# Kernel tuning notes

Hardware: AMD Instinct MI355X
Metric: run time of the kernel (lower is better)

## Reference

```python
import jax, jax.numpy as jnp
import numpy as np

B, S, H, D = 4, 2048, 16, 64
DM = H * D  # d_model = 1024


def setup_inputs() -> dict:
    key = jax.random.key(0)
    ks = jax.random.split(key, 11)
    s = 1.0 / np.sqrt(DM)
    return {
        "query": jax.random.normal(ks[0], (B, S, DM), jnp.float32),
        "key": jax.random.normal(ks[1], (B, S, DM), jnp.float32),
        "value": jax.random.normal(ks[2], (B, S, DM), jnp.float32),
        "Wq": jax.random.uniform(ks[3], (DM, DM), jnp.float32, -s, s),
        "bq": jax.random.uniform(ks[4], (DM,), jnp.float32, -s, s),
        "Wk": jax.random.uniform(ks[5], (DM, DM), jnp.float32, -s, s),
        "bk": jax.random.uniform(ks[6], (DM,), jnp.float32, -s, s),
        "Wv": jax.random.uniform(ks[7], (DM, DM), jnp.float32, -s, s),
        "bv": jax.random.uniform(ks[8], (DM,), jnp.float32, -s, s),
        "Wo": jax.random.uniform(ks[9], (DM, DM), jnp.float32, -s, s),
        "bo": jax.random.uniform(ks[10], (DM,), jnp.float32, -s, s),
        "masking": 1,
    }


def reference(query, key, value, Wq, bq, Wk, bk, Wv, bv, Wo, bo, masking):
    b, s, _ = query.shape
    # Linear projections (torch Linear: x @ W.T + b), split into heads
    q = (query @ Wq.T + bq).reshape(b, s, H, D).transpose(0, 2, 1, 3)  # [B,H,S,D]
    k = (key @ Wk.T + bk).reshape(b, -1, H, D).transpose(0, 2, 1, 3)
    v = (value @ Wv.T + bv).reshape(b, -1, H, D).transpose(0, 2, 1, 3)
    scores = jnp.einsum("bhqd,bhkd->bhqk", q, k) / np.power(D, 0.5)
    if masking:
        # subsequent (strictly upper-triangular) mask -> fill with -1e9
        sub = jnp.triu(jnp.ones((s, k.shape[2]), bool), k=1)
        scores = jnp.where(sub, jnp.float32(-1e9), scores)
    attn = jax.nn.softmax(scores, axis=-1)
    out = jnp.einsum("bhqk,bhkd->bhqd", attn, v)  # [B,H,S,D]
    out = out.transpose(0, 2, 1, 3).reshape(b, s, H * D)
    return out @ Wo.T + bo
```

## Files before the change

### kernel.cpp

```cpp
#include <hip/hip_runtime.h>
#include <stdint.h>
#include <stddef.h>

#define B_ 4
#define S_ 2048
#define H_ 16
#define D_ 64
#define DM 1024
#define MTOT 8192

typedef __bf16 bf16x8 __attribute__((ext_vector_type(8)));
typedef __bf16 bf16x4 __attribute__((ext_vector_type(4)));
typedef float  f32x4  __attribute__((ext_vector_type(4)));

__device__ __forceinline__ void g2l16(const void* g, void* l) {
  __builtin_amdgcn_global_load_lds(
      (__attribute__((address_space(1))) void*)g,
      (__attribute__((address_space(3))) void*)l, 16, 0, 0);
}

__global__ __launch_bounds__(256) void cvt_kernel(const float* __restrict__ src,
                                                  __bf16* __restrict__ dst, int n4) {
  int i = blockIdx.x * 256 + threadIdx.x;
  if (i < n4) {
    const float4 v = ((const float4*)src)[i];
    bf16x4 o;
    o.x = (__bf16)v.x; o.y = (__bf16)v.y; o.z = (__bf16)v.z; o.w = (__bf16)v.w;
    ((bf16x4*)dst)[i] = o;
  }
}

struct QKVArgs {
  const __bf16 *A0, *A1, *A2;
  const __bf16 *W0, *W1, *W2;
  const float *b0, *b1, *b2;
  __bf16 *oQ, *oK, *oVt;
};

__global__ __launch_bounds__(256) void gemm_qkv(QKVArgs args) {
  const int z = blockIdx.z;
  const __bf16* A    = (z == 0) ? args.A0 : (z == 1) ? args.A1 : args.A2;
  const __bf16* W    = (z == 0) ? args.W0 : (z == 1) ? args.W1 : args.W2;
  const float*  bias = (z == 0) ? args.b0 : (z == 1) ? args.b1 : args.b2;

  __shared__ __bf16 As[128 * 32];
  __shared__ __bf16 Bs[128 * 32];

  const int m0 = blockIdx.x * 128;
  const int n0 = blockIdx.y * 128;
  const int tid = threadIdx.x;
  const int wave = tid >> 6, lane = tid & 63;
  const int lrow = lane & 15, lhi = lane >> 4;
  const int moff = (wave & 1) * 64, noff = (wave >> 1) * 64;
  const int srow = lane >> 2;
  const int schunk = (lane & 3) * 8;

  f32x4 acc[4][4] = {};

  for (int k0 = 0; k0 < DM; k0 += 32) {
#pragma unroll
    for (int p = 0; p < 2; ++p) {
      const int rg = (p * 4 + wave) * 16;
      g2l16(A + (size_t)(m0 + rg + srow) * DM + k0 + schunk, As + rg * 32 + lane * 8);
      g2l16(W + (size_t)(n0 + rg + srow) * DM + k0 + schunk, Bs + rg * 32 + lane * 8);
    }
    __syncthreads();
    bf16x8 af[4], bfr[4];
#pragma unroll
    for (int i = 0; i < 4; ++i) {
      af[i]  = *(const bf16x8*)(As + (moff + i * 16 + lrow) * 32 + lhi * 8);
      bfr[i] = *(const bf16x8*)(Bs + (noff + i * 16 + lrow) * 32 + lhi * 8);
    }
#pragma unroll
    for (int i = 0; i < 4; ++i)
#pragma unroll
      for (int j = 0; j < 4; ++j)
        acc[i][j] = __builtin_amdgcn_mfma_f32_16x16x32_bf16(af[i], bfr[j], acc[i][j], 0, 0, 0);
    __syncthreads();
  }

  if (z < 2) {
    __bf16* out = (z == 0) ? args.oQ : args.oK;
#pragma unroll
    for (int i = 0; i < 4; ++i)
#pragma unroll
      for (int j = 0; j < 4; ++j)
#pragma unroll
        for (int r = 0; r < 4; ++r) {
          const int row = m0 + moff + i * 16 + lhi * 4 + r;
          const int col = n0 + noff + j * 16 + lrow;
          out[(size_t)row * DM + col] = (__bf16)(acc[i][j][r] + bias[col]);
        }
  } else {
    __bf16* out = args.oVt;
#pragma unroll
    for (int i = 0; i < 4; ++i)
#pragma unroll
      for (int j = 0; j < 4; ++j)
#pragma unroll
        for (int r = 0; r < 4; ++r) {
          const int row = m0 + moff + i * 16 + lhi * 4 + r;
          const int col = n0 + noff + j * 16 + lrow;
          const int bb = row >> 11, s = row & 2047;
          const int hh = col >> 6,  d = col & 63;
          out[(((size_t)(bb * H_ + hh) * D_ + d) << 11) + s] =
              (__bf16)(acc[i][j][r] + bias[col]);
        }
  }
}

__global__ __launch_bounds__(256) void gemm_oproj(const __bf16* __restrict__ A,
                                                  const __bf16* __restrict__ W,
                                                  const float* __restrict__ bias,
                                                  float* __restrict__ out) {
  __shared__ __bf16 As[128 * 32];
  __shared__ __bf16 Bs[128 * 32];

  const int m0 = blockIdx.x * 128;
  const int n0 = blockIdx.y * 128;
  const int tid = threadIdx.x;
  const int wave = tid >> 6, lane = tid & 63;
  const int lrow = lane & 15, lhi = lane >> 4;
  const int moff = (wave & 1) * 64, noff = (wave >> 1) * 64;
  const int srow = lane >> 2;
  const int schunk = (lane & 3) * 8;

  f32x4 acc[4][4] = {};

  for (int k0 = 0; k0 < DM; k0 += 32) {
#pragma unroll
    for (int p = 0; p < 2; ++p) {
      const int rg = (p * 4 + wave) * 16;
      g2l16(A + (size_t)(m0 + rg + srow) * DM + k0 + schunk, As + rg * 32 + lane * 8);
      g2l16(W + (size_t)(n0 + rg + srow) * DM + k0 + schunk, Bs + rg * 32 + lane * 8);
    }
    __syncthreads();
    bf16x8 af[4], bfr[4];
#pragma unroll
    for (int i = 0; i < 4; ++i) {
      af[i]  = *(const bf16x8*)(As + (moff + i * 16 + lrow) * 32 + lhi * 8);
      bfr[i] = *(const bf16x8*)(Bs + (noff + i * 16 + lrow) * 32 + lhi * 8);
    }
#pragma unroll
    for (int i = 0; i < 4; ++i)
#pragma unroll
      for (int j = 0; j < 4; ++j)
        acc[i][j] = __builtin_amdgcn_mfma_f32_16x16x32_bf16(af[i], bfr[j], acc[i][j], 0, 0, 0);
    __syncthreads();
  }

#pragma unroll
  for (int i = 0; i < 4; ++i)
#pragma unroll
    for (int j = 0; j < 4; ++j)
#pragma unroll
      for (int r = 0; r < 4; ++r) {
        const int row = m0 + moff + i * 16 + lhi * 4 + r;
        const int col = n0 + noff + j * 16 + lrow;
        out[(size_t)row * DM + col] = acc[i][j][r] + bias[col];
      }
}

__global__ __launch_bounds__(256, 3) void attn_kernel(const __bf16* __restrict__ Q,
                                                      const __bf16* __restrict__ K,
                                                      const __bf16* __restrict__ Vt,
                                                      __bf16* __restrict__ O) {
  const int id = blockIdx.x;
  const int xcd = id & 7;
  const int tmp = id >> 3;
  const int tt = tmp & 15;
  const int bh = ((tmp >> 4) << 3) | xcd;
  const int t = 15 - tt;
  const int b = bh >> 4, h = bh & 15;

  const int wave = threadIdx.x >> 6;
  const int lane = threadIdx.x & 63;
  const int lrow = lane & 15, lhi = lane >> 4;
  const int qw0 = t * 128 + wave * 32;

  const __bf16* Qb = Q + (size_t)b * S_ * DM + h * D_;
  const __bf16* Kb = K + (size_t)b * S_ * DM + h * D_;
  const __bf16* Vb = Vt + (size_t)bh * D_ * S_;

  __shared__ __bf16 Ks[2][64 * 64];
  __shared__ __bf16 Vs[2][64 * 64];
  __shared__ __bf16 Ps[4][32 * 72];
  __bf16* const Pw = Ps[wave];

  bf16x8 qa[2][2];
#pragma unroll
  for (int m = 0; m < 2; ++m)
#pragma unroll
    for (int kd = 0; kd < 2; ++kd)
      qa[m][kd] = *(const bf16x8*)(Qb + (size_t)(qw0 + m * 16 + lrow) * DM + kd * 32 + lhi * 8);

  f32x4 o_acc[2][4] = {};
  float rs[2][4] = {};

  const int rl = lane >> 3;
  const int cg8 = ((lane & 7) ^ rl) * 8;
  const int jend = t * 128 + 64;

#pragma unroll
  for (int i = 0; i < 2; ++i) {
    const int row = wave * 16 + i * 8 + rl;
    g2l16(Kb + (size_t)row * DM + cg8, Ks[0] + ((wave * 16 + i * 8) << 6) + lane * 8);
    g2l16(Vb + (size_t)row * S_ + cg8, Vs[0] + ((wave * 16 + i * 8) << 6) + lane * 8);
  }

  int p = 0;
  for (int j0 = 0; j0 <= jend; j0 += 64) {
    __syncthreads();
    if (j0 < jend) {
      const int jn = j0 + 64;
#pragma unroll
      for (int i = 0; i < 2; ++i) {
        const int row = wave * 16 + i * 8 + rl;
        g2l16(Kb + (size_t)(jn + row) * DM + cg8, Ks[p ^ 1] + ((wave * 16 + i * 8) << 6) + lane * 8);
        g2l16(Vb + (size_t)row * S_ + jn + cg8, Vs[p ^ 1] + ((wave * 16 + i * 8) << 6) + lane * 8);
      }
    }

    bf16x8 kf[4][2];
#pragma unroll
    for (int kt = 0; kt < 4; ++kt) {
      const int r = kt * 16 + lrow;
#pragma unroll
      for (int kd = 0; kd < 2; ++kd)
        kf[kt][kd] = *(const bf16x8*)(Ks[p] + (r << 6) + (((kd * 4 + lhi) ^ (r & 7)) << 3));
    }
    f32x4 sc[2][4];
#pragma unroll
    for (int m = 0; m < 2; ++m)
#pragma unroll
      for (int kt = 0; kt < 4; ++kt) {
        f32x4 s = {};
        s = __builtin_amdgcn_mfma_f32_16x16x32_bf16(qa[m][0], kf[kt][0], s, 0, 0, 0);
        s = __builtin_amdgcn_mfma_f32_16x16x32_bf16(qa[m][1], kf[kt][1], s, 0, 0, 0);
        sc[m][kt] = s;
      }

    const bool diag = (j0 + 63 > qw0);
#pragma unroll
    for (int m = 0; m < 2; ++m)
#pragma unroll
      for (int kt = 0; kt < 4; ++kt)
#pragma unroll
        for (int r = 0; r < 4; ++r) {
          float v = sc[m][kt][r] * 0.1803368867f;
          if (diag && (j0 + kt * 16 + lrow > qw0 + m * 16 + lhi * 4 + r)) v = -1e9f;
          const float pv = exp2f(v);
          rs[m][r] += pv;
          Pw[(m * 16 + lhi * 4 + r) * 72 + kt * 16 + lrow] = (__bf16)pv;
        }

    bf16x8 vf[4][2];
#pragma unroll
    for (int dt = 0; dt < 4; ++dt) {
      const int r = dt * 16 + lrow;
#pragma unroll
      for (int kk = 0; kk < 2; ++kk)
        vf[dt][kk] = *(const bf16x8*)(Vs[p] + (r << 6) + (((kk * 4 + lhi) ^ (r & 7)) << 3));
    }
    bf16x8 pa[2][2];
#pragma unroll
    for (int m = 0; m < 2; ++m)
#pragma unroll
      for (int kk = 0; kk < 2; ++kk)
        pa[m][kk] = *(const bf16x8*)(Pw + (m * 16 + lrow) * 72 + kk * 32 + lhi * 8);
#pragma unroll
    for (int m = 0; m < 2; ++m)
#pragma unroll
      for (int dt = 0; dt < 4; ++dt) {
        o_acc[m][dt] = __builtin_amdgcn_mfma_f32_16x16x32_bf16(pa[m][0], vf[dt][0], o_acc[m][dt], 0, 0, 0);
        o_acc[m][dt] = __builtin_amdgcn_mfma_f32_16x16x32_bf16(pa[m][1], vf[dt][1], o_acc[m][dt], 0, 0, 0);
      }
    p ^= 1;
  }

#pragma unroll
  for (int off = 8; off >= 1; off >>= 1)
#pragma unroll
    for (int m = 0; m < 2; ++m)
#pragma unroll
      for (int r = 0; r < 4; ++r) rs[m][r] += __shfl_xor(rs[m][r], off);

#pragma unroll
  for (int m = 0; m < 2; ++m)
#pragma unroll
    for (int r = 0; r < 4; ++r) {
      const float inv = 1.0f / rs[m][r];
      const int qrow = qw0 + m * 16 + lhi * 4 + r;
      __bf16* orow = O + ((size_t)b * S_ + qrow) * DM + h * D_;
#pragma unroll
      for (int dt = 0; dt < 4; ++dt)
        orow[dt * 16 + lrow] = (__bf16)(o_acc[m][dt][r] * inv);
    }
}

extern "C" void kernel_launch(void* const* d_in, const int* in_sizes, int n_in,
                              void* d_out, int out_size, void* d_ws, size_t ws_size,
                              hipStream_t stream) {
  (void)in_sizes; (void)n_in; (void)out_size; (void)ws_size;
  const float* query = (const float*)d_in[0];
  const float* key   = (const float*)d_in[1];
  const float* value = (const float*)d_in[2];
  const float* Wq = (const float*)d_in[3];
  const float* bq = (const float*)d_in[4];
  const float* Wk = (const float*)d_in[5];
  const float* bk = (const float*)d_in[6];
  const float* Wv = (const float*)d_in[7];
  const float* bv = (const float*)d_in[8];
  const float* Wo = (const float*)d_in[9];
  const float* bo = (const float*)d_in[10];

  const size_t NX = (size_t)MTOT * DM;
  const size_t NW = (size_t)DM * DM;
  __bf16* p = (__bf16*)d_ws;
  __bf16 *Xq = p, *Xk = Xq + NX, *Xv = Xk + NX;
  __bf16 *Wqb = Xv + NX, *Wkb = Wqb + NW, *Wvb = Wkb + NW, *Wob = Wvb + NW;
  __bf16 *Qrm = Wob + NW, *Krm = Qrm + NX, *Vt = Krm + NX, *Orm = Vt + NX;

  const int nbx = (int)(NX / 4 / 256);
  const int nbw = (int)(NW / 4 / 256);
  cvt_kernel<<<nbx, 256, 0, stream>>>(query, Xq, (int)(NX / 4));
  cvt_kernel<<<nbx, 256, 0, stream>>>(key,   Xk, (int)(NX / 4));
  cvt_kernel<<<nbx, 256, 0, stream>>>(value, Xv, (int)(NX / 4));
  cvt_kernel<<<nbw, 256, 0, stream>>>(Wq, Wqb, (int)(NW / 4));
  cvt_kernel<<<nbw, 256, 0, stream>>>(Wk, Wkb, (int)(NW / 4));
  cvt_kernel<<<nbw, 256, 0, stream>>>(Wv, Wvb, (int)(NW / 4));
  cvt_kernel<<<nbw, 256, 0, stream>>>(Wo, Wob, (int)(NW / 4));

  QKVArgs qa;
  qa.A0 = Xq; qa.A1 = Xk; qa.A2 = Xv;
  qa.W0 = Wqb; qa.W1 = Wkb; qa.W2 = Wvb;
  qa.b0 = bq; qa.b1 = bk; qa.b2 = bv;
  qa.oQ = Qrm; qa.oK = Krm; qa.oVt = Vt;
  gemm_qkv<<<dim3(MTOT / 128, DM / 128, 3), 256, 0, stream>>>(qa);

  attn_kernel<<<dim3(1024), 256, 0, stream>>>(Qrm, Krm, Vt, Orm);

  gemm_oproj<<<dim3(MTOT / 128, DM / 128), 256, 0, stream>>>(Orm, Wob, bo, (float*)d_out);
}
```

Measured before the change: 386.2 us.

## Restructure attention: fold softmax scale into Wq, drop V LDS staging, transpose scores

Folds the softmax scale (1/sqrt(D)*log2e) into the bf16 Wq conversion and the Q bias, removing a multiply per score. The attention kernel now reads V fragments straight from global memory instead of staging them through LDS, computes scores transposed (K as the A operand) so each lane packs four P values into one swizzled bf16x4 LDS store, and reduces row sums with fewer shuffles. It also raises the occupancy hint to 4 blocks per CU and interleaves causal tile order across blocks for load balance. The trade-offs are uncached global V reads per wave and bf16 rounding of the pre-scaled weights.

Result: slower. 497.5 us (+28.8%).

```diff
diff --git a/kernel.cpp b/kernel.cpp
--- a/kernel.cpp
+++ b/kernel.cpp
@@ -8,6 +8,7 @@
 #define D_ 64
 #define DM 1024
 #define MTOT 8192
+#define QSCALE 0.1803368867f
 
 typedef __bf16 bf16x8 __attribute__((ext_vector_type(8)));
 typedef __bf16 bf16x4 __attribute__((ext_vector_type(4)));
@@ -20,12 +21,14 @@
 }
 
 __global__ __launch_bounds__(256) void cvt_kernel(const float* __restrict__ src,
-                                                  __bf16* __restrict__ dst, int n4) {
+                                                  __bf16* __restrict__ dst, int n4,
+                                                  float scale) {
   int i = blockIdx.x * 256 + threadIdx.x;
   if (i < n4) {
     const float4 v = ((const float4*)src)[i];
     bf16x4 o;
-    o.x = (__bf16)v.x; o.y = (__bf16)v.y; o.z = (__bf16)v.z; o.w = (__bf16)v.w;
+    o.x = (__bf16)(v.x * scale); o.y = (__bf16)(v.y * scale);
+    o.z = (__bf16)(v.z * scale); o.w = (__bf16)(v.w * scale);
     ((bf16x4*)dst)[i] = o;
   }
 }
@@ -42,6 +45,7 @@
   const __bf16* A    = (z == 0) ? args.A0 : (z == 1) ? args.A1 : args.A2;
   const __bf16* W    = (z == 0) ? args.W0 : (z == 1) ? args.W1 : args.W2;
   const float*  bias = (z == 0) ? args.b0 : (z == 1) ? args.b1 : args.b2;
+  const float   bsc  = (z == 0) ? QSCALE : 1.0f;
 
   __shared__ __bf16 As[128 * 32];
   __shared__ __bf16 Bs[128 * 32];
@@ -89,7 +93,7 @@
         for (int r = 0; r < 4; ++r) {
           const int row = m0 + moff + i * 16 + lhi * 4 + r;
           const int col = n0 + noff + j * 16 + lrow;
-          out[(size_t)row * DM + col] = (__bf16)(acc[i][j][r] + bias[col]);
+          out[(size_t)row * DM + col] = (__bf16)(acc[i][j][r] + bias[col] * bsc);
         }
   } else {
     __bf16* out = args.oVt;
@@ -161,7 +165,7 @@
       }
 }
 
-__global__ __launch_bounds__(256, 3) void attn_kernel(const __bf16* __restrict__ Q,
+__global__ __launch_bounds__(256, 4) void attn_kernel(const __bf16* __restrict__ Q,
                                                       const __bf16* __restrict__ K,
                                                       const __bf16* __restrict__ Vt,
                                                       __bf16* __restrict__ O) {
@@ -170,12 +174,13 @@
   const int tmp = id >> 3;
   const int tt = tmp & 15;
   const int bh = ((tmp >> 4) << 3) | xcd;
-  const int t = 15 - tt;
+  const int g = tt >> 2, j_ = tt & 3;
+  const int t = (g == 0) ? 15 - j_ : (g == 1) ? j_ : (g == 2) ? 11 - j_ : 4 + j_;
   const int b = bh >> 4, h = bh & 15;
 
   const int wave = threadIdx.x >> 6;
   const int lane = threadIdx.x & 63;
-  const int lrow = lane & 15, lhi = lane >> 4;
+  const int lq = lane & 15, lhi = lane >> 4;
   const int qw0 = t * 128 + wave * 32;
 
   const __bf16* Qb = Q + (size_t)b * S_ * DM + h * D_;
@@ -183,118 +188,116 @@
   const __bf16* Vb = Vt + (size_t)bh * D_ * S_;
 
   __shared__ __bf16 Ks[2][64 * 64];
-  __shared__ __bf16 Vs[2][64 * 64];
-  __shared__ __bf16 Ps[4][32 * 72];
+  __shared__ __bf16 Ps[4][32 * 64];
   __bf16* const Pw = Ps[wave];
 
-  bf16x8 qa[2][2];
+  bf16x8 qb[2][2];
 #pragma unroll
   for (int m = 0; m < 2; ++m)
 #pragma unroll
     for (int kd = 0; kd < 2; ++kd)
-      qa[m][kd] = *(const bf16x8*)(Qb + (size_t)(qw0 + m * 16 + lrow) * DM + kd * 32 + lhi * 8);
+      qb[m][kd] = *(const bf16x8*)(Qb + (size_t)(qw0 + m * 16 + lq) * DM + kd * 32 + lhi * 8);
 
   f32x4 o_acc[2][4] = {};
-  float rs[2][4] = {};
+  float rs[2] = {0.f, 0.f};
 
   const int rl = lane >> 3;
   const int cg8 = ((lane & 7) ^ rl) * 8;
   const int jend = t * 128 + 64;
 
 #pragma unroll
-  for (int i = 0; i < 2; ++i) {
-    const int row = wave * 16 + i * 8 + rl;
-    g2l16(Kb + (size_t)row * DM + cg8, Ks[0] + ((wave * 16 + i * 8) << 6) + lane * 8);
-    g2l16(Vb + (size_t)row * S_ + cg8, Vs[0] + ((wave * 16 + i * 8) << 6) + lane * 8);
-  }
+  for (int i = 0; i < 2; ++i)
+    g2l16(Kb + (size_t)(wave * 16 + i * 8 + rl) * DM + cg8,
+          Ks[0] + ((wave * 16 + i * 8) << 6) + lane * 8);
 
   int p = 0;
   for (int j0 = 0; j0 <= jend; j0 += 64) {
     __syncthreads();
     if (j0 < jend) {
-      const int jn = j0 + 64;
-#pragma unroll
-      for (int i = 0; i < 2; ++i) {
-        const int row = wave * 16 + i * 8 + rl;
-        g2l16(Kb + (size_t)(jn + row) * DM + cg8, Ks[p ^ 1] + ((wave * 16 + i * 8) << 6) + lane * 8);
-        g2l16(Vb + (size_t)row * S_ + jn + cg8, Vs[p ^ 1] + ((wave * 16 + i * 8) << 6) + lane * 8);
-      }
-    }
+#pragma unroll
+      for (int i = 0; i < 2; ++i)
+        g2l16(Kb + (size_t)(j0 + 64 + wave * 16 + i * 8 + rl) * DM + cg8,
+              Ks[p ^ 1] + ((wave * 16 + i * 8) << 6) + lane * 8);
+    }
+
+    bf16x8 vf[4][2];
+#pragma unroll
+    for (int dt = 0; dt < 4; ++dt)
+#pragma unroll
+      for (int kk = 0; kk < 2; ++kk)
+        vf[dt][kk] = *(const bf16x8*)(Vb + (size_t)(dt * 16 + lq) * S_ + j0 + kk * 32 + lhi * 8);
 
     bf16x8 kf[4][2];
 #pragma unroll
     for (int kt = 0; kt < 4; ++kt) {
-      const int r = kt * 16 + lrow;
+      const int r = kt * 16 + lq;
 #pragma unroll
       for (int kd = 0; kd < 2; ++kd)
         kf[kt][kd] = *(const bf16x8*)(Ks[p] + (r << 6) + (((kd * 4 + lhi) ^ (r & 7)) << 3));
     }
+
     f32x4 sc[2][4];
 #pragma unroll
     for (int m = 0; m < 2; ++m)
 #pragma unroll
       for (int kt = 0; kt < 4; ++kt) {
         f32x4 s = {};
-        s = __builtin_amdgcn_mfma_f32_16x16x32_bf16(qa[m][0], kf[kt][0], s, 0, 0, 0);
-        s = __builtin_amdgcn_mfma_f32_16x16x32_bf16(qa[m][1], kf[kt][1], s, 0, 0, 0);
+        s = __builtin_amdgcn_mfma_f32_16x16x32_bf16(kf[kt][0], qb[m][0], s, 0, 0, 0);
+        s = __builtin_amdgcn_mfma_f32_16x16x32_bf16(kf[kt][1], qb[m][1], s, 0, 0, 0);
         sc[m][kt] = s;
       }
 
-    const bool diag = (j0 + 63 > qw0);
-#pragma unroll
-    for (int m = 0; m < 2; ++m)
-#pragma unroll
-      for (int kt = 0; kt < 4; ++kt)
+#pragma unroll
+    for (int m = 0; m < 2; ++m) {
+      const bool dg = (j0 + 63 > qw0 + m * 16);
+      const int thr = qw0 + m * 16 + lq - j0;
+#pragma unroll
+      for (int kt = 0; kt < 4; ++kt) {
+        bf16x4 pk;
 #pragma unroll
         for (int r = 0; r < 4; ++r) {
-          float v = sc[m][kt][r] * 0.1803368867f;
-          if (diag && (j0 + kt * 16 + lrow > qw0 + m * 16 + lhi * 4 + r)) v = -1e9f;
+          float v = sc[m][kt][r];
+          if (dg && (kt * 16 + lhi * 4 + r > thr)) v = -1e9f;
           const float pv = exp2f(v);
-          rs[m][r] += pv;
-          Pw[(m * 16 + lhi * 4 + r) * 72 + kt * 16 + lrow] = (__bf16)pv;
+          rs[m] += pv;
+          pk[r] = (__bf16)pv;
         }
-
-    bf16x8 vf[4][2];
-#pragma unroll
-    for (int dt = 0; dt < 4; ++dt) {
-      const int r = dt * 16 + lrow;
+        const int c = (kt * 2 + (lhi >> 1)) ^ (lq & 7);
+        *(bf16x4*)(Pw + ((m * 16 + lq) << 6) + (c << 3) + ((lhi & 1) << 2)) = pk;
+      }
+    }
+
+#pragma unroll
+    for (int m = 0; m < 2; ++m) {
+      bf16x8 pa[2];
 #pragma unroll
       for (int kk = 0; kk < 2; ++kk)
-        vf[dt][kk] = *(const bf16x8*)(Vs[p] + (r << 6) + (((kk * 4 + lhi) ^ (r & 7)) << 3));
-    }
-    bf16x8 pa[2][2];
-#pragma unroll
-    for (int m = 0; m < 2; ++m)
-#pragma unroll
-      for (int kk = 0; kk < 2; ++kk)
-        pa[m][kk] = *(const bf16x8*)(Pw + (m * 16 + lrow) * 72 + kk * 32 + lhi * 8);
-#pragma unroll
-    for (int m = 0; m < 2; ++m)
+        pa[kk] = *(const bf16x8*)(Pw + ((m * 16 + lq) << 6) + ((((kk * 4) + lhi) ^ (lq & 7)) << 3));
 #pragma unroll
       for (int dt = 0; dt < 4; ++dt) {
-        o_acc[m][dt] = __builtin_amdgcn_mfma_f32_16x16x32_bf16(pa[m][0], vf[dt][0], o_acc[m][dt], 0, 0, 0);
-        o_acc[m][dt] = __builtin_amdgcn_mfma_f32_16x16x32_bf16(pa[m][1], vf[dt][1], o_acc[m][dt], 0, 0, 0);
+        o_acc[m][dt] = __builtin_amdgcn_mfma_f32_16x16x32_bf16(pa[0], vf[dt][0], o_acc[m][dt], 0, 0, 0);
+        o_acc[m][dt] = __builtin_amdgcn_mfma_f32_16x16x32_bf16(pa[1], vf[dt][1], o_acc[m][dt], 0, 0, 0);
       }
+    }
     p ^= 1;
   }
 
 #pragma unroll
-  for (int off = 8; off >= 1; off >>= 1)
-#pragma unroll
-    for (int m = 0; m < 2; ++m)
-#pragma unroll
-      for (int r = 0; r < 4; ++r) rs[m][r] += __shfl_xor(rs[m][r], off);
+  for (int m = 0; m < 2; ++m) {
+    rs[m] += __shfl_xor(rs[m], 16);
+    rs[m] += __shfl_xor(rs[m], 32);
+  }
 
 #pragma unroll
   for (int m = 0; m < 2; ++m)
 #pragma unroll
     for (int r = 0; r < 4; ++r) {
-      const float inv = 1.0f / rs[m][r];
+      const float inv = 1.0f / __shfl(rs[m], lhi * 4 + r);
       const int qrow = qw0 + m * 16 + lhi * 4 + r;
       __bf16* orow = O + ((size_t)b * S_ + qrow) * DM + h * D_;
 #pragma unroll
       for (int dt = 0; dt < 4; ++dt)
-        orow[dt * 16 + lrow] = (__bf16)(o_acc[m][dt][r] * inv);
+        orow[dt * 16 + lq] = (__bf16)(o_acc[m][dt][r] * inv);
     }
 }
 
@@ -323,13 +326,13 @@
 
   const int nbx = (int)(NX / 4 / 256);
   const int nbw = (int)(NW / 4 / 256);
-  cvt_kernel<<<nbx, 256, 0, stream>>>(query, Xq, (int)(NX / 4));
-  cvt_kernel<<<nbx, 256, 0, stream>>>(key,   Xk, (int)(NX / 4));
-  cvt_kernel<<<nbx, 256, 0, stream>>>(value, Xv, (int)(NX / 4));
-  cvt_kernel<<<nbw, 256, 0, stream>>>(Wq, Wqb, (int)(NW / 4));
-  cvt_kernel<<<nbw, 256, 0, stream>>>(Wk, Wkb, (int)(NW / 4));
-  cvt_kernel<<<nbw, 256, 0, stream>>>(Wv, Wvb, (int)(NW / 4));
-  cvt_kernel<<<nbw, 256, 0, stream>>>(Wo, Wob, (int)(NW / 4));
+  cvt_kernel<<<nbx, 256, 0, stream>>>(query, Xq, (int)(NX / 4), 1.0f);
+  cvt_kernel<<<nbx, 256, 0, stream>>>(key,   Xk, (int)(NX / 4), 1.0f);
+  cvt_kernel<<<nbx, 256, 0, stream>>>(value, Xv, (int)(NX / 4), 1.0f);
+  cvt_kernel<<<nbw, 256, 0, stream>>>(Wq, Wqb, (int)(NW / 4), QSCALE);
+  cvt_kernel<<<nbw, 256, 0, stream>>>(Wk, Wkb, (int)(NW / 4), 1.0f);
+  cvt_kernel<<<nbw, 256, 0, stream>>>(Wv, Wvb, (int)(NW / 4), 1.0f);
+  cvt_kernel<<<nbw, 256, 0, stream>>>(Wo, Wob, (int)(NW / 4), 1.0f);
 
   QKVArgs qa;
   qa.A0 = Xq; qa.A1 = Xk; qa.A2 = Xv;
```
